# Optimization experiments

Hardware: AMD Instinct MI355X
Metric: run time of the kernel (lower is better)

Reference implementation:

```python
import jax, jax.numpy as jnp
import numpy as np
from jax import lax

K = 5      # reassembly kernel
D = 2      # delta (downsample factor)


def _conv(x, w, b, stride=1, pad=0):
    y = lax.conv_general_dilated(x, w, (stride, stride), [(pad, pad), (pad, pad)],
                                 dimension_numbers=("NCHW", "OIHW", "NCHW"))
    return y + b[None, :, None, None]


def setup_inputs() -> dict:
    key = jax.random.key(0)
    ks = jax.random.split(key, 7)
    inC, outC, Cm = 64, 64, 64
    N, H, W = 2, 256, 256
    return {
        "x": jax.random.normal(ks[0], (N, inC, H, W), jnp.float32),
        "down_w": jax.random.normal(ks[1], (Cm, inC, 1, 1), jnp.float32) * 0.1,
        "down_b": jax.random.normal(ks[2], (Cm,), jnp.float32) * 0.1,
        "enc_w": jax.random.normal(ks[3], (K * K, Cm, 3, 3), jnp.float32) * 0.1,
        "enc_b": jax.random.normal(ks[4], (K * K,), jnp.float32) * 0.1,
        "out_w": jax.random.normal(ks[5], (outC, inC * D * D, 1, 1), jnp.float32) * 0.1,
        "out_b": jax.random.normal(ks[6], (outC,), jnp.float32) * 0.1,
    }


def reference(x, down_w, down_b, enc_w, enc_b, out_w, out_b):
    N, C, H, W = x.shape
    Hd, Wd = H // D, W // D
    p = K // 2

    # kernel prediction branch
    k = _conv(x, down_w, down_b)                       # (N, Cm, H, W)
    k = _conv(k, enc_w, enc_b, stride=D, pad=1)        # (N, K*K, Hd, Wd)
    k = jax.nn.softmax(k, axis=1)
    k = k.transpose(0, 2, 3, 1)                        # (N, Hd, Wd, K*K)

    # overlapping K x K windows at every (h, w): (N, C, H, W, K*K)
    xp = jnp.pad(x, ((0, 0), (0, 0), (p, p), (p, p)))
    patches = jnp.stack([xp[:, :, i:i + H, j:j + W]
                         for i in range(K) for j in range(K)], axis=-1)
    # faithful torch reshape (row-major reinterpretation, NOT space-to-depth)
    patches = patches.reshape(N, C * D * D, Hd, Wd, K * K)
    patches = patches.transpose(0, 2, 3, 1, 4)         # (N, Hd, Wd, C*D*D, K*K)

    out = jnp.einsum("nhwck,nhwk->nhwc", patches, k)   # weighted reassembly
    out = out.transpose(0, 3, 1, 2)                    # (N, C*D*D, Hd, Wd)
    return _conv(out, out_w, out_b)
```

## Files before the change

kernel.cpp:

```cpp
#include <hip/hip_runtime.h>
#include <hip/hip_bf16.h>

using u16 = unsigned short;
typedef __attribute__((ext_vector_type(8))) short bf16x8;
typedef __attribute__((ext_vector_type(4))) float f32x4;

static constexpr int N  = 2;
static constexpr int C  = 64;
static constexpr int H  = 256;
static constexpr int W  = 256;
static constexpr int Hd = 128;
static constexpr int Wd = 128;
static constexpr int KK = 25;
static constexpr int C2 = 256;
static constexpr int OC = 64;
static constexpr int HWP  = H * W;
static constexpr int HDWD = Hd * Wd;

__device__ __forceinline__ float bflo(unsigned u) { return __uint_as_float(u << 16); }
__device__ __forceinline__ float bfhi(unsigned u) { return __uint_as_float(u & 0xffff0000u); }
__device__ __forceinline__ unsigned pack2(float a, float b) {
    __hip_bfloat16 ha = __float2bfloat16(a), hb = __float2bfloat16(b);
    union { __hip_bfloat16 h; u16 u; } ua{ha}, ub{hb};
    return (unsigned)ua.u | ((unsigned)ub.u << 16);
}
__device__ __forceinline__ u16 f2bf(float f) {
    union { __hip_bfloat16 h; u16 u; } v{__float2bfloat16(f)};
    return v.u;
}

__global__ __launch_bounds__(256) void kA_down(const float* __restrict__ x,
                                               const float* __restrict__ w,
                                               const float* __restrict__ b,
                                               u16* __restrict__ k1) {
    __shared__ u16   xt[64][256];
    __shared__ float wt[64][66];
    const int tid = threadIdx.x;
    const int pg0 = blockIdx.x * 256;
    const int n   = pg0 >> 16;
    const int px0 = pg0 & (HWP - 1);

#pragma unroll
    for (int i = 0; i < 16; ++i) {
        int e  = i * 256 + tid;
        int cm = e >> 6, c = e & 63;
        wt[c][cm] = w[e];
    }
    const float* xb = x + (size_t)n * C * HWP + px0;
#pragma unroll
    for (int i = 0; i < 16; ++i) {
        int flat = i * 256 + tid;
        int row  = flat >> 6;
        int col4 = flat & 63;
        float4 v = *(const float4*)(xb + (size_t)row * HWP + col4 * 4);
        uint2 p;
        p.x = pack2(v.x, v.y);
        p.y = pack2(v.z, v.w);
        *(uint2*)&xt[row][col4 * 4] = p;
    }
    __syncthreads();

    const int cg  = tid & 7;
    const int pxg = tid >> 3;
    float acc[8][8];
#pragma unroll
    for (int j = 0; j < 8; ++j) {
        float bj = b[cg * 8 + j];
#pragma unroll
        for (int p = 0; p < 8; ++p) acc[j][p] = bj;
    }
#pragma unroll 8
    for (int c = 0; c < 64; ++c) {
        uint4 xv = *(const uint4*)&xt[c][pxg * 8];
        float xs[8] = {bflo(xv.x), bfhi(xv.x), bflo(xv.y), bfhi(xv.y),
                       bflo(xv.z), bfhi(xv.z), bflo(xv.w), bfhi(xv.w)};
        float2 w01 = *(const float2*)&wt[c][cg * 8 + 0];
        float2 w23 = *(const float2*)&wt[c][cg * 8 + 2];
        float2 w45 = *(const float2*)&wt[c][cg * 8 + 4];
        float2 w67 = *(const float2*)&wt[c][cg * 8 + 6];
        float wv[8] = {w01.x, w01.y, w23.x, w23.y, w45.x, w45.y, w67.x, w67.y};
#pragma unroll
        for (int j = 0; j < 8; ++j)
#pragma unroll
            for (int p = 0; p < 8; ++p) acc[j][p] = fmaf(wv[j], xs[p], acc[j][p]);
    }
#pragma unroll
    for (int p = 0; p < 8; ++p) {
        uint4 o;
        o.x = pack2(acc[0][p], acc[1][p]);
        o.y = pack2(acc[2][p], acc[3][p]);
        o.z = pack2(acc[4][p], acc[5][p]);
        o.w = pack2(acc[6][p], acc[7][p]);
        *(uint4*)(k1 + ((size_t)pg0 + pxg * 8 + p) * 64 + cg * 8) = o;
    }
}

__global__ __launch_bounds__(256) void kW2_pack(const float* __restrict__ ew,
                                                u16* __restrict__ bfr) {
    int idx = blockIdx.x * 256 + threadIdx.x;
    if (idx < 2304) {
        int l  = idx & 63;
        int ft = idx >> 6;
        int t  = ft & 1, s = ft >> 1;
        int tap = s >> 1, h = s & 1;
        int c = l & 15, q = l >> 4;
        int kk = t * 16 + c;
        u16 o[8];
#pragma unroll
        for (int j = 0; j < 8; ++j) {
            int cm = 32 * h + 8 * q + j;
            float v = (kk < 25) ? ew[(kk * 64 + cm) * 9 + tap] : 0.f;
            o[j] = f2bf(v);
        }
        *(uint4*)(bfr + (size_t)idx * 8) = *(uint4*)o;
    }
}

__global__ __launch_bounds__(256) void kB2_enc(const u16* __restrict__ k1,
                                               const u16* __restrict__ bfr,
                                               const float* __restrict__ eb,
                                               float* __restrict__ ksm) {
    __shared__ u16 tile[3 * 130 * 72];
    const int tid = threadIdx.x;
    const int b   = blockIdx.x;
    const int half = b & 1;
    const int hd   = (b >> 1) & 127;
    const int n    = b >> 8;
    const int w0 = half * 64;
    const int xb = 2 * w0 - 1;
    const int y0 = 2 * hd - 1;
    const u16* kb = k1 + (size_t)n * HWP * 64;

    for (int r = 0; r < 13; ++r) {
        int f = r * 256 + tid;
        if (f < 3096) {
            int p  = f >> 3, ch = f & 7;
            int y  = p / 129, xi = p - y * 129;
            int yy = y0 + y, xx = xb + xi;
            uint4 v = make_uint4(0u, 0u, 0u, 0u);
            if (yy >= 0 && xx >= 0 && xx < 256)
                v = *(const uint4*)(kb + ((size_t)(yy * W + xx)) * 64 + ch * 8);
            *(uint4*)&tile[(y * 130 + xi) * 72 + ch * 8] = v;
        }
    }
    __syncthreads();

    const int wv = tid >> 6;
    const int l  = tid & 63;
    const int c  = l & 15;
    const int q  = l >> 4;

    f32x4 acc0 = {0.f, 0.f, 0.f, 0.f};
    f32x4 acc1 = {0.f, 0.f, 0.f, 0.f};
#pragma unroll
    for (int s = 0; s < 18; ++s) {
        const int tap = s >> 1, h = s & 1;
        const int dy = tap / 3, dx = tap - dy * 3;
        const u16* ap = &tile[(dy * 130 + 32 * wv + 2 * c + dx) * 72 + 32 * h + 8 * q];
        bf16x8 a  = *(const bf16x8*)ap;
        bf16x8 b0 = *(const bf16x8*)(bfr + ((size_t)(s * 2 + 0) * 64 + l) * 8);
        bf16x8 b1 = *(const bf16x8*)(bfr + ((size_t)(s * 2 + 1) * 64 + l) * 8);
        acc0 = __builtin_amdgcn_mfma_f32_16x16x32_bf16(a, b0, acc0, 0, 0, 0);
        acc1 = __builtin_amdgcn_mfma_f32_16x16x32_bf16(a, b1, acc1, 0, 0, 0);
    }

    const float e0 = eb[c];
    const float e1 = eb[min(16 + c, 24)];
    const bool c9 = (c < 9);

#pragma unroll
    for (int r = 0; r < 4; ++r) {
        float l0 = acc0[r] + e0;
        float l1 = c9 ? (acc1[r] + e1) : -1e30f;
        float mx = fmaxf(l0, l1);
#pragma unroll
        for (int d = 1; d < 16; d <<= 1) mx = fmaxf(mx, __shfl_xor(mx, d, 64));
        float x0 = __expf(l0 - mx);
        float x1 = c9 ? __expf(l1 - mx) : 0.f;
        float sm = x0 + x1;
#pragma unroll
        for (int d = 1; d < 16; d <<= 1) sm += __shfl_xor(sm, d, 64);
        float inv = 1.f / sm;
        int wd = w0 + 16 * wv + q * 4 + r;
        float* op = ksm + (size_t)n * KK * HDWD + hd * Wd + wd;
        op[(size_t)c * HDWD] = x0 * inv;
        if (c9) op[(size_t)(16 + c) * HDWD] = x1 * inv;
    }
}

__global__ __launch_bounds__(256) void kC_reassemble(const float* __restrict__ x,
                                                     const float* __restrict__ ksm,
                                                     u16* __restrict__ out2) {
    __shared__ float xts[6 * 272];
    const int tid = threadIdx.x;
    const int b   = blockIdx.x;
    const int cchunk = b & 7;
    const int hdt = (b >> 3) & 31;
    const int q   = (b >> 8) & 3;
    const int n   = b >> 10;
    const int hd0 = hdt * 4;
    const int wv   = tid >> 6;
    const int lane = tid & 63;
    const int hd  = hd0 + wv;
    const int wd0 = lane * 2;
    const int w0  = ((wv & 1) << 7) + wd0;
    const int lr0 = wv >> 1;
    const int y0  = q * 64 + (hd0 >> 1) - 2;
    const int c0  = cchunk * 8;

    const float* kb = ksm + (size_t)n * KK * HDWD + hd * Wd + wd0;
    float2 kw[25];
#pragma unroll
    for (int kk = 0; kk < 25; ++kk) kw[kk] = *(const float2*)(kb + (size_t)kk * HDWD);

    const int s0 = tid, s1 = tid + 256;
    const int r0s = s0 / 68, c40 = s0 - r0s * 68;
    const int r1s = s1 / 68, c41 = s1 - r1s * 68;
    const int ya = y0 + r0s, yb = y0 + r1s;
    const bool v0 = (c40 >= 1) & (c40 <= 64) & (ya >= 0) & (ya < H);
    const bool v1 = (s1 < 408) & (c41 >= 1) & (c41 <= 64) & (yb >= 0) & (yb < H);
    const float* xn = x + (size_t)n * C * HWP + (size_t)c0 * HWP;
    const float* g0 = xn + (size_t)ya * W + (c40 - 1) * 4;
    const float* g1 = xn + (size_t)yb * W + (c41 - 1) * 4;

    const float4 z = make_float4(0.f, 0.f, 0.f, 0.f);
    float4 p0 = v0 ? *(const float4*)g0 : z;
    float4 p1 = v1 ? *(const float4*)g1 : z;

    for (int ci = 0; ci < 8; ++ci) {
        __syncthreads();
        *(float4*)&xts[4 * s0] = p0;
        if (s1 < 408) *(float4*)&xts[4 * s1] = p1;
        __syncthreads();

        if (ci < 7) {
            p0 = v0 ? *(const float4*)(g0 + (size_t)(ci + 1) * HWP) : z;
            p1 = v1 ? *(const float4*)(g1 + (size_t)(ci + 1) * HWP) : z;
        }

        float a0 = 0.f, a1 = 0.f;
#pragma unroll
        for (int i = 0; i < 5; ++i) {
            const float* rr = &xts[(lr0 + i) * 272 + w0 + 2];
            float2 r0 = *(const float2*)(rr + 0);
            float2 r1 = *(const float2*)(rr + 2);
            float2 r2 = *(const float2*)(rr + 4);
            float f[6] = {r0.x, r0.y, r1.x, r1.y, r2.x, r2.y};
#pragma unroll
            for (int j = 0; j < 5; ++j) {
                const float2 kv = kw[i * 5 + j];
                a0 = fmaf(f[j + 0], kv.x, a0);
                a1 = fmaf(f[j + 1], kv.y, a1);
            }
        }
        const int c2 = 4 * (c0 + ci) + q;
        u16* op = out2 + ((size_t)(n * C2 + c2) * Hd + hd) * Wd + wd0;
        *(unsigned*)op = pack2(a0, a1);
    }
}

__global__ __launch_bounds__(256) void kD_out(const u16* __restrict__ out2,
                                              const float* __restrict__ ow,
                                              const float* __restrict__ ob,
                                              float* __restrict__ out) {
    const int co0 = blockIdx.y * 4;
    const int pg  = blockIdx.x * 256 + threadIdx.x;
    const int n   = pg >> 12;
    const int hw  = (pg << 2) & (HDWD - 1);
    const u16* ib = out2 + (size_t)n * C2 * HDWD + hw;

    float acc[4][4];
#pragma unroll
    for (int j = 0; j < 4; ++j) {
        float bj = ob[co0 + j];
#pragma unroll
        for (int p = 0; p < 4; ++p) acc[j][p] = bj;
    }
    for (int c2 = 0; c2 < 256; c2 += 8) {
        uint2 u[8];
#pragma unroll
        for (int t = 0; t < 8; ++t)
            u[t] = *(const uint2*)(ib + (size_t)(c2 + t) * HDWD);
#pragma unroll
        for (int t = 0; t < 8; ++t) {
            float xs[4] = {bflo(u[t].x), bfhi(u[t].x), bflo(u[t].y), bfhi(u[t].y)};
#pragma unroll
            for (int j = 0; j < 4; ++j) {
                float wv = ow[(co0 + j) * 256 + c2 + t];
#pragma unroll
                for (int p = 0; p < 4; ++p) acc[j][p] = fmaf(wv, xs[p], acc[j][p]);
            }
        }
    }
#pragma unroll
    for (int j = 0; j < 4; ++j) {
        float* op = out + (size_t)(n * OC + co0 + j) * HDWD + hw;
        *(float4*)op = make_float4(acc[j][0], acc[j][1], acc[j][2], acc[j][3]);
    }
}

extern "C" void kernel_launch(void* const* d_in, const int* in_sizes, int n_in,
                              void* d_out, int out_size, void* d_ws, size_t ws_size,
                              hipStream_t stream) {
    const float* x  = (const float*)d_in[0];
    const float* dw = (const float*)d_in[1];
    const float* db = (const float*)d_in[2];
    const float* ew = (const float*)d_in[3];
    const float* eb = (const float*)d_in[4];
    const float* ow = (const float*)d_in[5];
    const float* ob = (const float*)d_in[6];
    float* out = (float*)d_out;

    char* ws = (char*)d_ws;
    u16*   k1   = (u16*)ws;
    float* ksm  = (float*)(ws + 16777216);
    u16*   out2 = (u16*)(ws + 16777216 + 3276800);
    u16*   bfr  = out2;

    kW2_pack<<<dim3(9), dim3(256), 0, stream>>>(ew, bfr);
    kA_down<<<dim3(512), dim3(256), 0, stream>>>(x, dw, db, k1);
    kB2_enc<<<dim3(512), dim3(256), 0, stream>>>(k1, bfr, eb, ksm);
    kC_reassemble<<<dim3(2048), dim3(256), 0, stream>>>(x, ksm, out2);
    kD_out<<<dim3(32, 16), dim3(256), 0, stream>>>(out2, ow, ob, out);
}
```

Baseline: 164.8 us.

## Use MFMA for output 1x1 conv with channel-last reassembly output

The final 1x1 conv moves from scalar FMAs to bf16 MFMA 16x16x32 instructions. Its weights are pre-packed into MFMA fragment layout, and the reassembly kernel now writes its intermediate in pixel-major, channel-contiguous layout so A fragments load as contiguous vectors. The reassembly kernel computes all four row strips per block, loading 4 channels at a time into shared memory. The down-projection kernel halves its pixels per block to launch more blocks. The weight pack reuses the k1 workspace after the encoder has consumed it, and the intermediate writes become scattered 16-element channel chunks.

```diff
diff --git a/kernel.cpp b/kernel.cpp
--- a/kernel.cpp
+++ b/kernel.cpp
@@ -33,10 +33,10 @@
                                                const float* __restrict__ w,
                                                const float* __restrict__ b,
                                                u16* __restrict__ k1) {
-    __shared__ u16   xt[64][256];
+    __shared__ u16   xt[64][128];
     __shared__ float wt[64][66];
     const int tid = threadIdx.x;
-    const int pg0 = blockIdx.x * 256;
+    const int pg0 = blockIdx.x * 128;
     const int n   = pg0 >> 16;
     const int px0 = pg0 & (HWP - 1);
 
@@ -48,10 +48,10 @@
     }
     const float* xb = x + (size_t)n * C * HWP + px0;
 #pragma unroll
-    for (int i = 0; i < 16; ++i) {
+    for (int i = 0; i < 8; ++i) {
         int flat = i * 256 + tid;
-        int row  = flat >> 6;
-        int col4 = flat & 63;
+        int row  = flat >> 5;
+        int col4 = flat & 31;
         float4 v = *(const float4*)(xb + (size_t)row * HWP + col4 * 4);
         uint2 p;
         p.x = pack2(v.x, v.y);
@@ -62,18 +62,17 @@
 
     const int cg  = tid & 7;
     const int pxg = tid >> 3;
-    float acc[8][8];
+    float acc[8][4];
 #pragma unroll
     for (int j = 0; j < 8; ++j) {
         float bj = b[cg * 8 + j];
 #pragma unroll
-        for (int p = 0; p < 8; ++p) acc[j][p] = bj;
+        for (int p = 0; p < 4; ++p) acc[j][p] = bj;
     }
 #pragma unroll 8
     for (int c = 0; c < 64; ++c) {
-        uint4 xv = *(const uint4*)&xt[c][pxg * 8];
-        float xs[8] = {bflo(xv.x), bfhi(xv.x), bflo(xv.y), bfhi(xv.y),
-                       bflo(xv.z), bfhi(xv.z), bflo(xv.w), bfhi(xv.w)};
+        uint2 xv = *(const uint2*)&xt[c][pxg * 4];
+        float xs[4] = {bflo(xv.x), bfhi(xv.x), bflo(xv.y), bfhi(xv.y)};
         float2 w01 = *(const float2*)&wt[c][cg * 8 + 0];
         float2 w23 = *(const float2*)&wt[c][cg * 8 + 2];
         float2 w45 = *(const float2*)&wt[c][cg * 8 + 4];
@@ -82,16 +81,16 @@
 #pragma unroll
         for (int j = 0; j < 8; ++j)
 #pragma unroll
-            for (int p = 0; p < 8; ++p) acc[j][p] = fmaf(wv[j], xs[p], acc[j][p]);
-    }
-#pragma unroll
-    for (int p = 0; p < 8; ++p) {
+            for (int p = 0; p < 4; ++p) acc[j][p] = fmaf(wv[j], xs[p], acc[j][p]);
+    }
+#pragma unroll
+    for (int p = 0; p < 4; ++p) {
         uint4 o;
         o.x = pack2(acc[0][p], acc[1][p]);
         o.y = pack2(acc[2][p], acc[3][p]);
         o.z = pack2(acc[4][p], acc[5][p]);
         o.w = pack2(acc[6][p], acc[7][p]);
-        *(uint4*)(k1 + ((size_t)pg0 + pxg * 8 + p) * 64 + cg * 8) = o;
+        *(uint4*)(k1 + ((size_t)pg0 + pxg * 4 + p) * 64 + cg * 8) = o;
     }
 }
 
@@ -113,6 +112,23 @@
             o[j] = f2bf(v);
         }
         *(uint4*)(bfr + (size_t)idx * 8) = *(uint4*)o;
+    }
+}
+
+__global__ __launch_bounds__(256) void kW3_pack(const float* __restrict__ ow,
+                                                u16* __restrict__ bfr2) {
+    int idx = blockIdx.x * 256 + threadIdx.x;
+    if (idx < 2048) {
+        int l  = idx & 63;
+        int ft = idx >> 6;
+        int nt = ft & 3, s = ft >> 2;
+        int c = l & 15, q = l >> 4;
+        int co = nt * 16 + c;
+        u16 o[8];
+#pragma unroll
+        for (int j = 0; j < 8; ++j)
+            o[j] = f2bf(ow[co * 256 + s * 32 + q * 8 + j]);
+        *(uint4*)(bfr2 + (size_t)idx * 8) = *(uint4*)o;
     }
 }
 
@@ -188,115 +204,134 @@
     }
 }
 
-__global__ __launch_bounds__(256) void kC_reassemble(const float* __restrict__ x,
-                                                     const float* __restrict__ ksm,
-                                                     u16* __restrict__ out2) {
-    __shared__ float xts[6 * 272];
+__global__ __launch_bounds__(256) void kC2_reassemble(const float* __restrict__ x,
+                                                      const float* __restrict__ ksm,
+                                                      u16* __restrict__ out2p) {
+    __shared__ float xts[4 * 6 * 272];
     const int tid = threadIdx.x;
     const int b   = blockIdx.x;
-    const int cchunk = b & 7;
-    const int hdt = (b >> 3) & 31;
-    const int q   = (b >> 8) & 3;
-    const int n   = b >> 10;
+    const int cc  = b & 15;
+    const int hdt = (b >> 4) & 31;
+    const int n   = b >> 9;
     const int hd0 = hdt * 4;
-    const int wv   = tid >> 6;
-    const int lane = tid & 63;
-    const int hd  = hd0 + wv;
-    const int wd0 = lane * 2;
-    const int w0  = ((wv & 1) << 7) + wd0;
-    const int lr0 = wv >> 1;
-    const int y0  = q * 64 + (hd0 >> 1) - 2;
-    const int c0  = cchunk * 8;
+    const int hdo = tid >> 6;
+    const int wdg = tid & 63;
+    const int hd  = hd0 + hdo;
+    const int wd0 = wdg * 2;
+    const int w0  = ((hdo & 1) << 7) + wd0;
+    const int lr0 = hdo >> 1;
+    const int c0  = cc * 4;
 
     const float* kb = ksm + (size_t)n * KK * HDWD + hd * Wd + wd0;
     float2 kw[25];
 #pragma unroll
     for (int kk = 0; kk < 25; ++kk) kw[kk] = *(const float2*)(kb + (size_t)kk * HDWD);
 
-    const int s0 = tid, s1 = tid + 256;
-    const int r0s = s0 / 68, c40 = s0 - r0s * 68;
-    const int r1s = s1 / 68, c41 = s1 - r1s * 68;
-    const int ya = y0 + r0s, yb = y0 + r1s;
-    const bool v0 = (c40 >= 1) & (c40 <= 64) & (ya >= 0) & (ya < H);
-    const bool v1 = (s1 < 408) & (c41 >= 1) & (c41 <= 64) & (yb >= 0) & (yb < H);
-    const float* xn = x + (size_t)n * C * HWP + (size_t)c0 * HWP;
-    const float* g0 = xn + (size_t)ya * W + (c40 - 1) * 4;
-    const float* g1 = xn + (size_t)yb * W + (c41 - 1) * 4;
-
+    int  soff[7];
+    bool sval[7];
+#pragma unroll
+    for (int k = 0; k < 7; ++k) {
+        int s = tid + 256 * k;
+        int strip = s / 408;
+        int rem   = s - 408 * strip;
+        int r     = rem / 68;
+        int c4    = rem - 68 * r;
+        int y     = strip * 64 + (hd0 >> 1) - 2 + r;
+        sval[k] = (s < 1632) & (c4 >= 1) & (c4 <= 64) & (y >= 0) & (y < H);
+        int yc  = min(max(y, 0), H - 1);
+        soff[k] = yc * W + (c4 - 1) * 4;
+    }
+
+    unsigned o0[8], o1[8];
     const float4 z = make_float4(0.f, 0.f, 0.f, 0.f);
-    float4 p0 = v0 ? *(const float4*)g0 : z;
-    float4 p1 = v1 ? *(const float4*)g1 : z;
-
-    for (int ci = 0; ci < 8; ++ci) {
+
+#pragma unroll
+    for (int ci = 0; ci < 4; ++ci) {
         __syncthreads();
-        *(float4*)&xts[4 * s0] = p0;
-        if (s1 < 408) *(float4*)&xts[4 * s1] = p1;
+        const float* base = x + (size_t)(n * C + c0 + ci) * HWP;
+#pragma unroll
+        for (int k = 0; k < 7; ++k) {
+            int s = tid + 256 * k;
+            if (s < 1632) {
+                float4 v = sval[k] ? *(const float4*)(base + soff[k]) : z;
+                *(float4*)&xts[4 * s] = v;
+            }
+        }
         __syncthreads();
 
-        if (ci < 7) {
-            p0 = v0 ? *(const float4*)(g0 + (size_t)(ci + 1) * HWP) : z;
-            p1 = v1 ? *(const float4*)(g1 + (size_t)(ci + 1) * HWP) : z;
-        }
-
-        float a0 = 0.f, a1 = 0.f;
-#pragma unroll
-        for (int i = 0; i < 5; ++i) {
-            const float* rr = &xts[(lr0 + i) * 272 + w0 + 2];
-            float2 r0 = *(const float2*)(rr + 0);
-            float2 r1 = *(const float2*)(rr + 2);
-            float2 r2 = *(const float2*)(rr + 4);
-            float f[6] = {r0.x, r0.y, r1.x, r1.y, r2.x, r2.y};
-#pragma unroll
-            for (int j = 0; j < 5; ++j) {
-                const float2 kv = kw[i * 5 + j];
-                a0 = fmaf(f[j + 0], kv.x, a0);
-                a1 = fmaf(f[j + 1], kv.y, a1);
+#pragma unroll
+        for (int q = 0; q < 4; ++q) {
+            float a0 = 0.f, a1 = 0.f;
+#pragma unroll
+            for (int i = 0; i < 5; ++i) {
+                const float* rr = &xts[(q * 6 + lr0 + i) * 272 + w0 + 2];
+                float2 r0 = *(const float2*)(rr + 0);
+                float2 r1 = *(const float2*)(rr + 2);
+                float2 r2 = *(const float2*)(rr + 4);
+                float f[6] = {r0.x, r0.y, r1.x, r1.y, r2.x, r2.y};
+#pragma unroll
+                for (int j = 0; j < 5; ++j) {
+                    const float2 kv = kw[i * 5 + j];
+                    a0 = fmaf(f[j + 0], kv.x, a0);
+                    a1 = fmaf(f[j + 1], kv.y, a1);
+                }
             }
-        }
-        const int c2 = 4 * (c0 + ci) + q;
-        u16* op = out2 + ((size_t)(n * C2 + c2) * Hd + hd) * Wd + wd0;
-        *(unsigned*)op = pack2(a0, a1);
-    }
-}
-
-__global__ __launch_bounds__(256) void kD_out(const u16* __restrict__ out2,
-                                              const float* __restrict__ ow,
-                                              const float* __restrict__ ob,
-                                              float* __restrict__ out) {
-    const int co0 = blockIdx.y * 4;
-    const int pg  = blockIdx.x * 256 + threadIdx.x;
-    const int n   = pg >> 12;
-    const int hw  = (pg << 2) & (HDWD - 1);
-    const u16* ib = out2 + (size_t)n * C2 * HDWD + hw;
-
-    float acc[4][4];
-#pragma unroll
-    for (int j = 0; j < 4; ++j) {
-        float bj = ob[co0 + j];
-#pragma unroll
-        for (int p = 0; p < 4; ++p) acc[j][p] = bj;
-    }
-    for (int c2 = 0; c2 < 256; c2 += 8) {
-        uint2 u[8];
-#pragma unroll
-        for (int t = 0; t < 8; ++t)
-            u[t] = *(const uint2*)(ib + (size_t)(c2 + t) * HDWD);
-#pragma unroll
-        for (int t = 0; t < 8; ++t) {
-            float xs[4] = {bflo(u[t].x), bfhi(u[t].x), bflo(u[t].y), bfhi(u[t].y)};
-#pragma unroll
-            for (int j = 0; j < 4; ++j) {
-                float wv = ow[(co0 + j) * 256 + c2 + t];
-#pragma unroll
-                for (int p = 0; p < 4; ++p) acc[j][p] = fmaf(wv, xs[p], acc[j][p]);
+            const int idx  = 4 * ci + q;
+            const int word = idx >> 1;
+            if ((idx & 1) == 0) {
+                o0[word] = (unsigned)f2bf(a0);
+                o1[word] = (unsigned)f2bf(a1);
+            } else {
+                o0[word] |= ((unsigned)f2bf(a0)) << 16;
+                o1[word] |= ((unsigned)f2bf(a1)) << 16;
             }
         }
     }
-#pragma unroll
-    for (int j = 0; j < 4; ++j) {
-        float* op = out + (size_t)(n * OC + co0 + j) * HDWD + hw;
-        *(float4*)op = make_float4(acc[j][0], acc[j][1], acc[j][2], acc[j][3]);
-    }
+
+    u16* p0 = out2p + ((size_t)(n * HDWD + hd * Wd + wd0)) * 256 + cc * 16;
+    *(uint4*)(p0 + 0) = make_uint4(o0[0], o0[1], o0[2], o0[3]);
+    *(uint4*)(p0 + 8) = make_uint4(o0[4], o0[5], o0[6], o0[7]);
+    u16* p1 = p0 + 256;
+    *(uint4*)(p1 + 0) = make_uint4(o1[0], o1[1], o1[2], o1[3]);
+    *(uint4*)(p1 + 8) = make_uint4(o1[4], o1[5], o1[6], o1[7]);
+}
+
+__global__ __launch_bounds__(256) void kD2_out(const u16* __restrict__ out2p,
+                                               const u16* __restrict__ bfr2,
+                                               const float* __restrict__ ob,
+                                               float* __restrict__ out) {
+    const int tid = threadIdx.x;
+    const int b   = blockIdx.x;
+    const int px0g = b * 64;
+    const int n    = px0g >> 14;
+    const int px0  = px0g & (HDWD - 1);
+    const int nt = tid >> 6;
+    const int l  = tid & 63;
+    const int c  = l & 15;
+    const int q  = l >> 4;
+
+    const u16* A = out2p + (size_t)px0g * 256;
+
+    f32x4 acc[4] = {{0.f,0.f,0.f,0.f},{0.f,0.f,0.f,0.f},
+                    {0.f,0.f,0.f,0.f},{0.f,0.f,0.f,0.f}};
+#pragma unroll
+    for (int s = 0; s < 8; ++s) {
+        bf16x8 bf = *(const bf16x8*)(bfr2 + ((size_t)(s * 4 + nt) * 64 + l) * 8);
+#pragma unroll
+        for (int mt = 0; mt < 4; ++mt) {
+            const u16* ap = A + ((size_t)(mt * 16 + c)) * 256 + s * 32 + q * 8;
+            bf16x8 a = *(const bf16x8*)ap;
+            acc[mt] = __builtin_amdgcn_mfma_f32_16x16x32_bf16(a, bf, acc[mt], 0, 0, 0);
+        }
+    }
+    const int co = nt * 16 + c;
+    const float bias = ob[co];
+    float* ob_ = out + (size_t)(n * OC + co) * HDWD + px0;
+#pragma unroll
+    for (int mt = 0; mt < 4; ++mt)
+#pragma unroll
+        for (int r = 0; r < 4; ++r)
+            ob_[mt * 16 + q * 4 + r] = acc[mt][r] + bias;
 }
 
 extern "C" void kernel_launch(void* const* d_in, const int* in_sizes, int n_in,
@@ -312,14 +347,16 @@
     float* out = (float*)d_out;
 
     char* ws = (char*)d_ws;
-    u16*   k1   = (u16*)ws;
-    float* ksm  = (float*)(ws + 16777216);
-    u16*   out2 = (u16*)(ws + 16777216 + 3276800);
-    u16*   bfr  = out2;
-
-    kW2_pack<<<dim3(9), dim3(256), 0, stream>>>(ew, bfr);
-    kA_down<<<dim3(512), dim3(256), 0, stream>>>(x, dw, db, k1);
-    kB2_enc<<<dim3(512), dim3(256), 0, stream>>>(k1, bfr, eb, ksm);
-    kC_reassemble<<<dim3(2048), dim3(256), 0, stream>>>(x, ksm, out2);
-    kD_out<<<dim3(32, 16), dim3(256), 0, stream>>>(out2, ow, ob, out);
-}
+    u16*   k1    = (u16*)ws;
+    float* ksm   = (float*)(ws + 16777216);
+    u16*   out2p = (u16*)(ws + 16777216 + 3276800);
+    u16*   bfr   = out2p;
+    u16*   bfr2  = k1;
+
+    kW2_pack<<<dim3(9),    dim3(256), 0, stream>>>(ew, bfr);
+    kA_down <<<dim3(1024), dim3(256), 0, stream>>>(x, dw, db, k1);
+    kB2_enc <<<dim3(512),  dim3(256), 0, stream>>>(k1, bfr, eb, ksm);
+    kW3_pack<<<dim3(8),    dim3(256), 0, stream>>>(ow, bfr2);
+    kC2_reassemble<<<dim3(1024), dim3(256), 0, stream>>>(x, ksm, out2p);
+    kD2_out <<<dim3(512),  dim3(256), 0, stream>>>(out2p, bfr2, ob, out);
+}
```

Result: slower. 180.7 us (+9.6%).
